# Kernel tuning notes

Measured on AMD Instinct MI355X. Metric: run time of the kernel, lower is better.

The kernel has to match this reference:

```python
import jax, jax.numpy as jnp
import numpy as np

HIDDEN = 128
NUM_FILTERS = 128
NUM_RBF = 50
NUM_LAYERS = 3
MAX_Z = 100
CUTOFF_LO, CUTOFF_HI = 0.0, 5.0
N_ATOMS = 10000
N_EDGES = 320000


def _xavier(k, shape):
    fan_out, fan_in = shape[-2], shape[-1]
    a = (6.0 / (fan_in + fan_out)) ** 0.5
    return jax.random.uniform(k, shape, jnp.float32, -a, a)


def setup_inputs() -> dict:
    key = jax.random.key(0)
    ks = jax.random.split(key, 16)
    start = float(np.exp(-CUTOFF_HI + CUTOFF_LO))  # ExpNormalSmearing start value
    L = NUM_LAYERS
    return {
        "z": jax.random.randint(ks[0], (N_ATOMS,), 0, MAX_Z),
        "edge_index": jax.random.randint(ks[1], (2, N_EDGES), 0, N_ATOMS),
        "edge_weight": jax.random.uniform(ks[2], (N_EDGES,), jnp.float32, 0.0, CUTOFF_HI),
        "emb_table": jax.random.normal(ks[3], (MAX_Z, HIDDEN), jnp.float32),
        "means": jnp.linspace(start, 1.0, NUM_RBF, dtype=jnp.float32),
        "betas": jnp.full((NUM_RBF,), (2.0 / NUM_RBF * (1.0 - start)) ** -2, dtype=jnp.float32),
        "ne_proj_w": _xavier(ks[4], (HIDDEN, NUM_RBF)),
        "ne_proj_b": jnp.zeros((HIDDEN,), jnp.float32),
        "ne_comb_w": _xavier(ks[5], (HIDDEN, 2 * HIDDEN)),
        "ne_comb_b": jnp.zeros((HIDDEN,), jnp.float32),
        "mlp_w0": _xavier(ks[6], (L, NUM_FILTERS, NUM_RBF)),
        "mlp_b0": jnp.zeros((L, NUM_FILTERS), jnp.float32),
        "mlp_w1": _xavier(ks[7], (L, NUM_FILTERS, NUM_FILTERS)),
        "mlp_b1": jnp.zeros((L, NUM_FILTERS), jnp.float32),
        "lin1_w": _xavier(ks[8], (L, NUM_FILTERS, HIDDEN)),
        "lin2_w": _xavier(ks[9], (L, HIDDEN, NUM_FILTERS)),
        "lin2_b": jnp.zeros((L, HIDDEN), jnp.float32),
        "lin_w": _xavier(ks[10], (L, HIDDEN, HIDDEN)),
        "lin_b": jnp.zeros((L, HIDDEN), jnp.float32),
    }


def _cosine_cutoff(d):
    c = 0.5 * (jnp.cos(d * (jnp.pi / CUTOFF_HI)) + 1.0)
    return jnp.where(d < CUTOFF_HI, c, 0.0)


def reference(z, edge_index, edge_weight, emb_table, means, betas,
              ne_proj_w, ne_proj_b, ne_comb_w, ne_comb_b,
              mlp_w0, mlp_b0, mlp_w1, mlp_b1, lin1_w, lin2_w, lin2_b, lin_w, lin_b):
    n_atoms = z.shape[0]
    src, dst = edge_index[0], edge_index[1]
    alpha = 5.0 / (CUTOFF_HI - CUTOFF_LO)
    C = _cosine_cutoff(edge_weight)  # [E]
    # ExpNormalSmearing (includes cutoff factor)
    rbf = jnp.exp(-betas * (jnp.exp(alpha * (CUTOFF_LO - edge_weight))[:, None] - means) ** 2)
    edge_attr = C[:, None] * rbf  # [E, NUM_RBF]

    x = emb_table[z]  # [N, H]

    # NeighborEmbedding (self loops masked out, as in the original)
    mask = (src != dst)[:, None]
    W = (edge_attr @ ne_proj_w.T + ne_proj_b) * C[:, None]
    W = jnp.where(mask, W, 0.0)
    agg = jax.ops.segment_sum(W * emb_table[z][dst], src, num_segments=n_atoms)
    x = jnp.concatenate([x, agg], axis=1) @ ne_comb_w.T + ne_comb_b

    def layer(xc, p):
        w0, b0, w1, b1, l1w, l2w, l2b, lw, lb = p
        # filter network: MLP(edge_attr) * cutoff
        Wf = (jax.nn.silu(edge_attr @ w0.T + b0) @ w1.T + b1) * C[:, None]  # [E, F]
        h = xc @ l1w.T                                   # lin1 (no bias) [N, F]
        a = jax.ops.segment_sum(Wf * h[dst], src, num_segments=n_atoms)  # scatter-add
        h = jax.nn.silu(a @ l2w.T + l2b)                 # lin2 + act
        h = h @ lw.T + lb                                # final linear
        return xc + h, None

    x, _ = jax.lax.scan(layer, x, (mlp_w0, mlp_b0, mlp_w1, mlp_b1, lin1_w, lin2_w, lin2_b, lin_w, lin_b))
    return x
```

## Files before the change

### kernel.cpp

```cpp
#include <hip/hip_runtime.h>
#include <hip/hip_bf16.h>

#define NATOMS 10000
#define NEDGES 320000
#define H 128
#define NRBF 50
#define NELEM (NATOMS * H)
#define NT 4096

typedef unsigned short u16;
typedef unsigned int u32;
typedef __attribute__((ext_vector_type(8))) short short8;
typedef __attribute__((ext_vector_type(4))) float float4v;

__device__ __forceinline__ float bfu(u16 u) { return __uint_as_float(((u32)u) << 16); }
__device__ __forceinline__ u16 bf16r(float v) {
    u32 u = __float_as_uint(v);
    return (u16)((u + 0x7FFFu + ((u >> 16) & 1u)) >> 16);
}
__device__ __forceinline__ float ldf(const void* p, int i, int bf) {
    return bf ? bfu(((const u16*)p)[i]) : ((const float*)p)[i];
}
__device__ __forceinline__ float silu_f(float v) { return v / (1.f + __expf(-v)); }
__device__ __forceinline__ int bfflag(const void* means) {
    return ((((const u32*)means)[24] >> 16) == 0x3F80u) ? 1 : 0;
}

__global__ __launch_bounds__(256) void k_embed(const int* __restrict__ z, const void* emb,
                                               const void* means,
                                               float* __restrict__ x0, u16* __restrict__ xh,
                                               int* __restrict__ degz,
                                               float* __restrict__ zb) {
    int bf = bfflag(means);
    int i = blockIdx.x * 256 + threadIdx.x;
    if (i < 20480) degz[i] = 0;
    if (i < NELEM / 4) ((float4*)zb)[i] = make_float4(0.f, 0.f, 0.f, 0.f);
    if (i < NELEM) {
        int n = i >> 7, f = i & 127;
        float v = ldf(emb, z[n] * H + f, bf);
        x0[i] = v;
        xh[i] = bf16r(v);
    }
}

__device__ __forceinline__ void stage_w16(const void* W, int woff, int wstride,
                                          u16* sW, int tid, int nthr, int bf) {
    u32* sW32 = (u32*)sW;
    if (bf) {
        const u32* W32 = (const u32*)W;
        for (int i = tid; i < 128 * 64; i += nthr) {
            int f2 = i >> 6, kk = i & 63;
            sW32[f2 * 68 + kk] = W32[((woff + f2 * wstride) >> 1) + kk];
        }
    } else {
        const float2* Wf = (const float2*)W;
        for (int i = tid; i < 128 * 64; i += nthr) {
            int f2 = i >> 6, kk = i & 63;
            float2 v = Wf[((woff + f2 * wstride) >> 1) + kk];
            sW32[f2 * 68 + kk] = (u32)bf16r(v.x) | ((u32)bf16r(v.y) << 16);
        }
    }
}

__global__ __launch_bounds__(256) void k_mfma_lin(const float* in,
                                                  const void* W2, int w2off,
                                                  const void* B2, int b2off,
                                                  const void* Wl, int wloff,
                                                  const void* Bl, int bloff,
                                                  const void* W1n, int w1noff,
                                                  float* x, u16* __restrict__ hb,
                                                  const void* means,
                                                  float* zrw, void* outp) {
    __shared__ u16 sW2[128 * 136];
    __shared__ u16 sWl[128 * 136];
    __shared__ u16 sW1[128 * 136];
    __shared__ u16 sA[4][16 * 136];
    __shared__ float sB2v[128], sBlv[128];
    int tid = threadIdx.x;
    int bf = bfflag(means);
    stage_w16(W2, w2off, H, sW2, tid, 256, bf);
    stage_w16(Wl, wloff, H, sWl, tid, 256, bf);
    if (W1n) stage_w16(W1n, w1noff, H, sW1, tid, 256, bf);
    if (tid < 128) {
        sB2v[tid] = ldf(B2, b2off + tid, bf);
        sBlv[tid] = ldf(Bl, bloff + tid, bf);
    }
    __syncthreads();
    int w = tid >> 6, lane = tid & 63;
    int quad = lane >> 4, l16 = lane & 15;
    u16* myA = sA[w];
    u32* myA32 = (u32*)myA;
    for (int tile = blockIdx.x * 4 + w; tile < NATOMS / 16; tile += gridDim.x * 4) {
        int abase = tile * 16;
        const float2* in2 = (const float2*)in + (size_t)abase * 64;
        #pragma unroll 4
        for (int j = 0; j < 16; ++j) {
            float2 v = in2[j * 64 + lane];
            myA32[j * 68 + lane] = (u32)bf16r(v.x) | ((u32)bf16r(v.y) << 16);
        }
        __asm__ volatile("s_waitcnt lgkmcnt(0)" ::: "memory");
        if (zrw) {
            float2* z2 = (float2*)zrw + (size_t)abase * 64;
            #pragma unroll 4
            for (int j = 0; j < 16; ++j) z2[j * 64 + lane] = make_float2(0.f, 0.f);
        }
        short8 af0 = *(const short8*)&myA[l16 * 136 +   0 + quad * 8];
        short8 af1 = *(const short8*)&myA[l16 * 136 +  32 + quad * 8];
        short8 af2 = *(const short8*)&myA[l16 * 136 +  64 + quad * 8];
        short8 af3 = *(const short8*)&myA[l16 * 136 +  96 + quad * 8];
        #pragma unroll 1
        for (int nt = 0; nt < 8; ++nt) {
            const u16* wrow = &sW2[(nt * 16 + l16) * 136];
            short8 b0 = *(const short8*)&wrow[0  + quad * 8];
            short8 b1 = *(const short8*)&wrow[32 + quad * 8];
            short8 b2 = *(const short8*)&wrow[64 + quad * 8];
            short8 b3 = *(const short8*)&wrow[96 + quad * 8];
            float4v acc = {0.f, 0.f, 0.f, 0.f};
            acc = __builtin_amdgcn_mfma_f32_16x16x32_bf16(af0, b0, acc, 0, 0, 0);
            acc = __builtin_amdgcn_mfma_f32_16x16x32_bf16(af1, b1, acc, 0, 0, 0);
            acc = __builtin_amdgcn_mfma_f32_16x16x32_bf16(af2, b2, acc, 0, 0, 0);
            acc = __builtin_amdgcn_mfma_f32_16x16x32_bf16(af3, b3, acc, 0, 0, 0);
            int col = nt * 16 + l16;
            float bias = sB2v[col];
            myA[(quad * 4 + 0) * 136 + col] = bf16r(silu_f(acc[0] + bias));
            myA[(quad * 4 + 1) * 136 + col] = bf16r(silu_f(acc[1] + bias));
            myA[(quad * 4 + 2) * 136 + col] = bf16r(silu_f(acc[2] + bias));
            myA[(quad * 4 + 3) * 136 + col] = bf16r(silu_f(acc[3] + bias));
        }
        __asm__ volatile("s_waitcnt lgkmcnt(0)" ::: "memory");
        short8 t0 = *(const short8*)&myA[l16 * 136 +   0 + quad * 8];
        short8 t1 = *(const short8*)&myA[l16 * 136 +  32 + quad * 8];
        short8 t2 = *(const short8*)&myA[l16 * 136 +  64 + quad * 8];
        short8 t3 = *(const short8*)&myA[l16 * 136 +  96 + quad * 8];
        #pragma unroll 1
        for (int nt = 0; nt < 8; ++nt) {
            const u16* wrow = &sWl[(nt * 16 + l16) * 136];
            short8 b0 = *(const short8*)&wrow[0  + quad * 8];
            short8 b1 = *(const short8*)&wrow[32 + quad * 8];
            short8 b2 = *(const short8*)&wrow[64 + quad * 8];
            short8 b3 = *(const short8*)&wrow[96 + quad * 8];
            int col = nt * 16 + l16;
            float bias = sBlv[col];
            float4v acc;
            acc[0] = x[(size_t)(abase + quad * 4 + 0) * H + col] + bias;
            acc[1] = x[(size_t)(abase + quad * 4 + 1) * H + col] + bias;
            acc[2] = x[(size_t)(abase + quad * 4 + 2) * H + col] + bias;
            acc[3] = x[(size_t)(abase + quad * 4 + 3) * H + col] + bias;
            acc = __builtin_amdgcn_mfma_f32_16x16x32_bf16(t0, b0, acc, 0, 0, 0);
            acc = __builtin_amdgcn_mfma_f32_16x16x32_bf16(t1, b1, acc, 0, 0, 0);
            acc = __builtin_amdgcn_mfma_f32_16x16x32_bf16(t2, b2, acc, 0, 0, 0);
            acc = __builtin_amdgcn_mfma_f32_16x16x32_bf16(t3, b3, acc, 0, 0, 0);
            #pragma unroll
            for (int r = 0; r < 4; ++r) {
                size_t idx = (size_t)(abase + quad * 4 + r) * H + col;
                x[idx] = acc[r];
                myA[(quad * 4 + r) * 136 + col] = bf16r(acc[r]);
                if (outp) {
                    if (bf) ((u16*)outp)[idx] = bf16r(acc[r]);
                    else    ((float*)outp)[idx] = acc[r];
                }
            }
        }
        if (W1n) {
            __asm__ volatile("s_waitcnt lgkmcnt(0)" ::: "memory");
            short8 h0 = *(const short8*)&myA[l16 * 136 +   0 + quad * 8];
            short8 h1 = *(const short8*)&myA[l16 * 136 +  32 + quad * 8];
            short8 h2 = *(const short8*)&myA[l16 * 136 +  64 + quad * 8];
            short8 h3 = *(const short8*)&myA[l16 * 136 +  96 + quad * 8];
            #pragma unroll 1
            for (int nt = 0; nt < 8; ++nt) {
                const u16* wrow = &sW1[(nt * 16 + l16) * 136];
                short8 b0 = *(const short8*)&wrow[0  + quad * 8];
                short8 b1 = *(const short8*)&wrow[32 + quad * 8];
                short8 b2 = *(const short8*)&wrow[64 + quad * 8];
                short8 b3 = *(const short8*)&wrow[96 + quad * 8];
                float4v acc = {0.f, 0.f, 0.f, 0.f};
                acc = __builtin_amdgcn_mfma_f32_16x16x32_bf16(h0, b0, acc, 0, 0, 0);
                acc = __builtin_amdgcn_mfma_f32_16x16x32_bf16(h1, b1, acc, 0, 0, 0);
                acc = __builtin_amdgcn_mfma_f32_16x16x32_bf16(h2, b2, acc, 0, 0, 0);
                acc = __builtin_amdgcn_mfma_f32_16x16x32_bf16(h3, b3, acc, 0, 0, 0);
                int col = nt * 16 + l16;
                hb[(size_t)(abase + quad * 4 + 0) * H + col] = bf16r(acc[0]);
                hb[(size_t)(abase + quad * 4 + 1) * H + col] = bf16r(acc[1]);
                hb[(size_t)(abase + quad * 4 + 2) * H + col] = bf16r(acc[2]);
                hb[(size_t)(abase + quad * 4 + 3) * H + col] = bf16r(acc[3]);
            }
        }
    }
}

__global__ __launch_bounds__(256) void k_mfma_comb(const float* in0, float* in1,
                                                   const void* W, const void* B,
                                                   const void* W1,
                                                   float* x, u16* __restrict__ hb,
                                                   const void* means) {
    __shared__ u16 sWa[128 * 136];
    __shared__ u16 sWb[128 * 136];
    __shared__ u16 sW1[128 * 136];
    __shared__ u16 sA[4][16 * 136];
    __shared__ float sBv[128];
    int tid = threadIdx.x;
    int bf = bfflag(means);
    stage_w16(W, 0,   256, sWa, tid, 256, bf);
    stage_w16(W, 128, 256, sWb, tid, 256, bf);
    stage_w16(W1, 0, H, sW1, tid, 256, bf);
    if (tid < 128) sBv[tid] = ldf(B, tid, bf);
    __syncthreads();
    int w = tid >> 6, lane = tid & 63;
    int quad = lane >> 4, l16 = lane & 15;
    u16* myA = sA[w];
    u32* myA32 = (u32*)myA;
    for (int tile = blockIdx.x * 4 + w; tile < NATOMS / 16; tile += gridDim.x * 4) {
        int abase = tile * 16;
        const float2* i0 = (const float2*)in0 + (size_t)abase * 64;
        const float2* i1 = (const float2*)in1 + (size_t)abase * 64;
        #pragma unroll 4
        for (int j = 0; j < 16; ++j) {
            float2 v = i0[j * 64 + lane];
            myA32[j * 68 + lane] = (u32)bf16r(v.x) | ((u32)bf16r(v.y) << 16);
        }
        __asm__ volatile("s_waitcnt lgkmcnt(0)" ::: "memory");
        short8 af0 = *(const short8*)&myA[l16 * 136 +   0 + quad * 8];
        short8 af1 = *(const short8*)&myA[l16 * 136 +  32 + quad * 8];
        short8 af2 = *(const short8*)&myA[l16 * 136 +  64 + quad * 8];
        short8 af3 = *(const short8*)&myA[l16 * 136 +  96 + quad * 8];
        #pragma unroll 4
        for (int j = 0; j < 16; ++j) {
            float2 v = i1[j * 64 + lane];
            myA32[j * 68 + lane] = (u32)bf16r(v.x) | ((u32)bf16r(v.y) << 16);
        }
        __asm__ volatile("s_waitcnt lgkmcnt(0)" ::: "memory");
        {
            float2* z2 = (float2*)in1 + (size_t)abase * 64;
            #pragma unroll 4
            for (int j = 0; j < 16; ++j) z2[j * 64 + lane] = make_float2(0.f, 0.f);
        }
        short8 ag0 = *(const short8*)&myA[l16 * 136 +   0 + quad * 8];
        short8 ag1 = *(const short8*)&myA[l16 * 136 +  32 + quad * 8];
        short8 ag2 = *(const short8*)&myA[l16 * 136 +  64 + quad * 8];
        short8 ag3 = *(const short8*)&myA[l16 * 136 +  96 + quad * 8];
        #pragma unroll 1
        for (int nt = 0; nt < 8; ++nt) {
            const u16* wra = &sWa[(nt * 16 + l16) * 136];
            const u16* wrb = &sWb[(nt * 16 + l16) * 136];
            int col = nt * 16 + l16;
            float bias = sBv[col];
            float4v acc = {bias, bias, bias, bias};
            acc = __builtin_amdgcn_mfma_f32_16x16x32_bf16(af0, *(const short8*)&wra[0  + quad * 8], acc, 0, 0, 0);
            acc = __builtin_amdgcn_mfma_f32_16x16x32_bf16(af1, *(const short8*)&wra[32 + quad * 8], acc, 0, 0, 0);
            acc = __builtin_amdgcn_mfma_f32_16x16x32_bf16(af2, *(const short8*)&wra[64 + quad * 8], acc, 0, 0, 0);
            acc = __builtin_amdgcn_mfma_f32_16x16x32_bf16(af3, *(const short8*)&wra[96 + quad * 8], acc, 0, 0, 0);
            acc = __builtin_amdgcn_mfma_f32_16x16x32_bf16(ag0, *(const short8*)&wrb[0  + quad * 8], acc, 0, 0, 0);
            acc = __builtin_amdgcn_mfma_f32_16x16x32_bf16(ag1, *(const short8*)&wrb[32 + quad * 8], acc, 0, 0, 0);
            acc = __builtin_amdgcn_mfma_f32_16x16x32_bf16(ag2, *(const short8*)&wrb[64 + quad * 8], acc, 0, 0, 0);
            acc = __builtin_amdgcn_mfma_f32_16x16x32_bf16(ag3, *(const short8*)&wrb[96 + quad * 8], acc, 0, 0, 0);
            #pragma unroll
            for (int r = 0; r < 4; ++r) {
                x[(size_t)(abase + quad * 4 + r) * H + col] = acc[r];
                myA[(quad * 4 + r) * 136 + col] = bf16r(acc[r]);
            }
        }
        __asm__ volatile("s_waitcnt lgkmcnt(0)" ::: "memory");
        short8 h0 = *(const short8*)&myA[l16 * 136 +   0 + quad * 8];
        short8 h1 = *(const short8*)&myA[l16 * 136 +  32 + quad * 8];
        short8 h2 = *(const short8*)&myA[l16 * 136 +  64 + quad * 8];
        short8 h3 = *(const short8*)&myA[l16 * 136 +  96 + quad * 8];
        #pragma unroll 1
        for (int nt = 0; nt < 8; ++nt) {
            const u16* wrow = &sW1[(nt * 16 + l16) * 136];
            short8 b0 = *(const short8*)&wrow[0  + quad * 8];
            short8 b1 = *(const short8*)&wrow[32 + quad * 8];
            short8 b2 = *(const short8*)&wrow[64 + quad * 8];
            short8 b3 = *(const short8*)&wrow[96 + quad * 8];
            float4v acc = {0.f, 0.f, 0.f, 0.f};
            acc = __builtin_amdgcn_mfma_f32_16x16x32_bf16(h0, b0, acc, 0, 0, 0);
            acc = __builtin_amdgcn_mfma_f32_16x16x32_bf16(h1, b1, acc, 0, 0, 0);
            acc = __builtin_amdgcn_mfma_f32_16x16x32_bf16(h2, b2, acc, 0, 0, 0);
            acc = __builtin_amdgcn_mfma_f32_16x16x32_bf16(h3, b3, acc, 0, 0, 0);
            int col = nt * 16 + l16;
            hb[(size_t)(abase + quad * 4 + 0) * H + col] = bf16r(acc[0]);
            hb[(size_t)(abase + quad * 4 + 1) * H + col] = bf16r(acc[1]);
            hb[(size_t)(abase + quad * 4 + 2) * H + col] = bf16r(acc[2]);
            hb[(size_t)(abase + quad * 4 + 3) * H + col] = bf16r(acc[3]);
        }
    }
}

__global__ __launch_bounds__(1024) void k_ft4(const void* means, const void* betas,
                                              const void* W0s, const void* B0s,
                                              const void* W1s, const void* B1s,
                                              const void* Wne, const void* Bne,
                                              u16* __restrict__ ftT,
                                              u16* __restrict__ Tne) {
    __shared__ float sW0[H * 53];
    __shared__ u16 sW1b[128 * 136];
    __shared__ u16 sA16[16 * 136];
    __shared__ float sR[16][56];
    __shared__ float sM[NRBF], sBe[NRBF], sB1v[128], sC[16];
    int tid = threadIdx.x;
    int bf = bfflag(means);
    int t = blockIdx.x >> 8;
    int bb = blockIdx.x & 255;
    int ne = (t == 3);
    const void* W0 = ne ? Wne : W0s;
    int w0off = ne ? 0 : t * H * NRBF;
    u16* T = ne ? Tne : (ftT + (size_t)t * NT * H);
    if (!ne) stage_w16(W1s, t * H * H, H, sW1b, tid, 1024, bf);
    for (int i = tid; i < H * NRBF; i += 1024) {
        int f2 = i / NRBF, k = i - f2 * NRBF;
        sW0[f2 * 53 + k] = ldf(W0, w0off + i, bf);
    }
    if (tid < NRBF) { sM[tid] = ldf(means, tid, bf); sBe[tid] = ldf(betas, tid, bf); }
    if (tid < 128) sB1v[tid] = ne ? 0.f : ldf(B1s, t * H + tid, bf);
    __syncthreads();
    int g = tid >> 7, f = tid & 127;
    float b0r = ne ? ldf(Bne, f, bf) : ldf(B0s, t * H + f, bf);
    int base = bb * 16;
    int n0 = base + 2 * g, n1 = n0 + 1;
    float wv0 = (float)n0 * (5.0f / (NT - 1));
    float wv1 = (float)n1 * (5.0f / (NT - 1));
    if (f < NRBF) {
        float tt = expf(-wv0) - sM[f];
        sR[2 * g][f] = expf(-sBe[f] * tt * tt);
    } else if (f >= 64 && f < 64 + NRBF) {
        float tt = expf(-wv1) - sM[f - 64];
        sR[2 * g + 1][f - 64] = expf(-sBe[f - 64] * tt * tt);
    }
    __syncthreads();
    float c0 = 0.5f * (cosf(wv0 * 0.62831853071795864f) + 1.f); if (!(wv0 < 5.f)) c0 = 0.f;
    float c1 = 0.5f * (cosf(wv1 * 0.62831853071795864f) + 1.f); if (!(wv1 < 5.f)) c1 = 0.f;
    if (f == 0) { sC[2 * g] = c0; sC[2 * g + 1] = c1; }
    float s0 = 0.f, s1 = 0.f;
    #pragma unroll
    for (int k = 0; k < NRBF; ++k) {
        float wk = sW0[f * 53 + k];
        s0 = fmaf(wk, sR[2 * g][k], s0);
        s1 = fmaf(wk, sR[2 * g + 1][k], s1);
    }
    if (ne) {
        T[(size_t)n0 * H + f] = bf16r(fmaf(c0, s0, b0r) * c0);
        T[(size_t)n1 * H + f] = bf16r(fmaf(c1, s1, b0r) * c1);
        return;
    }
    sA16[(2 * g) * 136 + f]     = bf16r(silu_f(fmaf(c0, s0, b0r)));
    sA16[(2 * g + 1) * 136 + f] = bf16r(silu_f(fmaf(c1, s1, b0r)));
    __syncthreads();
    int w = tid >> 6;
    if (w < 8) {
        int lane = tid & 63;
        int quad = lane >> 4, l16 = lane & 15;
        short8 a0 = *(const short8*)&sA16[l16 * 136 +   0 + quad * 8];
        short8 a1 = *(const short8*)&sA16[l16 * 136 +  32 + quad * 8];
        short8 a2 = *(const short8*)&sA16[l16 * 136 +  64 + quad * 8];
        short8 a3 = *(const short8*)&sA16[l16 * 136 +  96 + quad * 8];
        const u16* wrow = &sW1b[(w * 16 + l16) * 136];
        short8 b0 = *(const short8*)&wrow[0  + quad * 8];
        short8 b1 = *(const short8*)&wrow[32 + quad * 8];
        short8 b2 = *(const short8*)&wrow[64 + quad * 8];
        short8 b3 = *(const short8*)&wrow[96 + quad * 8];
        float4v acc = {0.f, 0.f, 0.f, 0.f};
        acc = __builtin_amdgcn_mfma_f32_16x16x32_bf16(a0, b0, acc, 0, 0, 0);
        acc = __builtin_amdgcn_mfma_f32_16x16x32_bf16(a1, b1, acc, 0, 0, 0);
        acc = __builtin_amdgcn_mfma_f32_16x16x32_bf16(a2, b2, acc, 0, 0, 0);
        acc = __builtin_amdgcn_mfma_f32_16x16x32_bf16(a3, b3, acc, 0, 0, 0);
        int col = w * 16 + l16;
        float bias = sB1v[col];
        #pragma unroll
        for (int r = 0; r < 4; ++r) {
            int row = quad * 4 + r;
            T[(size_t)(base + row) * H + col] = bf16r((acc[r] + bias) * sC[row]);
        }
    }
}

__global__ __launch_bounds__(256) void k_hist(const int* __restrict__ src, int* __restrict__ deg) {
    int e = blockIdx.x * 256 + threadIdx.x;
    if (e < NEDGES) atomicAdd(&deg[src[e]], 1);
}

__global__ __launch_bounds__(1024) void k_scan(const int* __restrict__ deg, int* __restrict__ rs) {
    __shared__ int wsum[16];
    int tid = threadIdx.x;
    int lane = tid & 63, w = tid >> 6;
    int d[10];
    int tot = 0;
    int base_i = tid * 10;
    if (tid < 1000) {
        #pragma unroll
        for (int j = 0; j < 10; ++j) d[j] = deg[base_i + j];
        #pragma unroll
        for (int j = 0; j < 10; ++j) { int v = d[j]; d[j] = tot; tot += v; }
    }
    int inc = tot;
    #pragma unroll
    for (int off = 1; off < 64; off <<= 1) {
        int n = __shfl_up(inc, off, 64);
        if (lane >= off) inc += n;
    }
    if (lane == 63) wsum[w] = inc;
    __syncthreads();
    if (w == 0) {
        int v = (lane < 16) ? wsum[lane] : 0;
        int vinc = v;
        #pragma unroll
        for (int off = 1; off < 16; off <<= 1) {
            int n = __shfl_up(vinc, off, 64);
            if (lane >= off) vinc += n;
        }
        if (lane < 16) wsum[lane] = vinc - v;
    }
    __syncthreads();
    if (tid < 1000) {
        int base = wsum[w] + (inc - tot);
        #pragma unroll
        for (int j = 0; j < 10; ++j) rs[base_i + j] = base + d[j];
    }
}

__global__ __launch_bounds__(256) void k_scatter_perm(const int* __restrict__ src,
                                                      const int* __restrict__ dst,
                                                      const void* ew, const void* means,
                                                      const int* __restrict__ rs,
                                                      int* __restrict__ cnt,
                                                      u32* __restrict__ sds,
                                                      float* __restrict__ ews) {
    int bf = bfflag(means);
    int e = blockIdx.x * 256 + threadIdx.x;
    if (e < NEDGES) {
        int s = src[e];
        int p = rs[s] + atomicAdd(&cnt[s], 1);
        sds[p] = (u32)s | ((u32)dst[e] << 14);
        ews[p] = ldf(ew, e, bf) * ((float)(NT - 1) / 5.0f);
    }
}

#define ELOAD(i) \
    u32 sd##i = sds[e + i]; \
    int s##i = (int)(sd##i & 16383u), d##i = (int)(sd##i >> 14); \
    float u##i = ews[e + i]; \
    int ix##i = min((int)u##i, NT - 2); float fr##i = u##i - (float)ix##i; \
    u32 ta##i = Tb[ix##i * 64 + lane], tb##i = Tb[ix##i * 64 + 64 + lane]; \
    u32 h##i = vh[d##i * 64 + lane];
#define EVAL(i) \
    float vx##i = fmaf(fr##i, bfu((u16)(tb##i & 0xffff)) - bfu((u16)(ta##i & 0xffff)), bfu((u16)(ta##i & 0xffff))) * bfu((u16)(h##i & 0xffff)); \
    float vy##i = fmaf(fr##i, bfu((u16)(tb##i >> 16))    - bfu((u16)(ta##i >> 16)),    bfu((u16)(ta##i >> 16)))    * bfu((u16)(h##i >> 16));
#define EACC(i) \
    if (!(mask_self && s##i == d##i)) { \
        if (s##i != cur) { \
            if (cur >= 0) { atomicAdd(&acc[cur * H + 2 * lane], rx); atomicAdd(&acc[cur * H + 2 * lane + 1], ry); } \
            cur = s##i; rx = 0.f; ry = 0.f; \
        } \
        rx += vx##i; ry += vy##i; \
    }

__global__ __launch_bounds__(256) void k_edge_apply4(const u32* __restrict__ sds,
                                                     const float* __restrict__ ews,
                                                     const u32* __restrict__ Tb,
                                                     const u32* __restrict__ vh,
                                                     float* __restrict__ acc,
                                                     int mask_self) {
    int tid = threadIdx.x;
    int g = tid >> 6;
    int lane = tid & 63;
    int gid = blockIdx.x * 4 + g;
    int r0 = gid * 40;
    int cur = -1;
    float rx = 0.f, ry = 0.f;
    for (int e = r0; e < r0 + 40; e += 8) {
        ELOAD(0) ELOAD(1) ELOAD(2) ELOAD(3) ELOAD(4) ELOAD(5) ELOAD(6) ELOAD(7)
        EVAL(0) EVAL(1) EVAL(2) EVAL(3) EVAL(4) EVAL(5) EVAL(6) EVAL(7)
        EACC(0) EACC(1) EACC(2) EACC(3) EACC(4) EACC(5) EACC(6) EACC(7)
    }
    if (cur >= 0) {
        atomicAdd(&acc[cur * H + 2 * lane], rx);
        atomicAdd(&acc[cur * H + 2 * lane + 1], ry);
    }
}

extern "C" void kernel_launch(void* const* d_in, const int* in_sizes, int n_in,
                              void* d_out, int out_size, void* d_ws, size_t ws_size,
                              hipStream_t stream) {
    const int* z  = (const int*)d_in[0];
    const int* ei = (const int*)d_in[1];
    const void* ew        = d_in[2];
    const void* emb       = d_in[3];
    const void* means     = d_in[4];
    const void* betas     = d_in[5];
    const void* ne_proj_w = d_in[6];
    const void* ne_proj_b = d_in[7];
    const void* ne_comb_w = d_in[8];
    const void* ne_comb_b = d_in[9];
    const void* mlp_w0    = d_in[10];
    const void* mlp_b0    = d_in[11];
    const void* mlp_w1    = d_in[12];
    const void* mlp_b1    = d_in[13];
    const void* lin1_w    = d_in[14];
    const void* lin2_w    = d_in[15];
    const void* lin2_b    = d_in[16];
    const void* lin_w     = d_in[17];
    const void* lin_b     = d_in[18];

    const int* srcp = ei;
    const int* dstp = ei + NEDGES;

    float* buf0 = (float*)d_ws;
    float* buf1 = buf0 + NELEM;
    float* x    = buf1 + NELEM;
    int*   deg  = (int*)(x + NELEM);
    int*   cnt  = deg + 10240;
    int*   rs   = cnt + 10240;
    u32*   sds  = (u32*)(rs + 10240);
    float* ews  = (float*)(sds + NEDGES);
    u16*   Tb   = (u16*)(ews + NEDGES);
    u16*   hb   = Tb + NT * H;
    u16*   ftT  = hb + NELEM;

    const int gElem = (NELEM + 255) / 256;
    const int gEdge = (NEDGES + 255) / 256;

    k_embed<<<gElem, 256, 0, stream>>>(z, emb, means, buf0, hb, deg, buf1);

    k_hist<<<gEdge, 256, 0, stream>>>(srcp, deg);
    k_scan<<<1, 1024, 0, stream>>>(deg, rs);
    k_scatter_perm<<<gEdge, 256, 0, stream>>>(srcp, dstp, ew, means, rs, cnt,
                                              sds, ews);

    k_ft4<<<1024, 1024, 0, stream>>>(means, betas, mlp_w0, mlp_b0, mlp_w1, mlp_b1,
                                     ne_proj_w, ne_proj_b, ftT, Tb);

    k_edge_apply4<<<2000, 256, 0, stream>>>(sds, ews, (const u32*)Tb,
                                            (const u32*)hb, buf1, 1);
    k_mfma_comb<<<157, 256, 0, stream>>>(buf0, buf1, ne_comb_w, ne_comb_b,
                                         lin1_w, x, hb, means);

    for (int L = 0; L < 3; ++L) {
        k_edge_apply4<<<2000, 256, 0, stream>>>(sds, ews,
                                                (const u32*)(ftT + (size_t)L * NT * H),
                                                (const u32*)hb, buf1, 0);
        k_mfma_lin<<<157, 256, 0, stream>>>(buf1, lin2_w, L * H * H, lin2_b, L * H,
                                            lin_w, L * H * H, lin_b, L * H,
                                            (L < 2) ? lin1_w : nullptr, (L + 1) * H * H,
                                            x, hb, means,
                                            (L < 2) ? buf1 : nullptr,
                                            (L == 2) ? d_out : nullptr);
    }
}
```

Baseline: 344.3 us.

## Replace atomic edge scatter with per-atom CSR gather writing bf16 aggregates

The edge kernel now assigns one wavefront per source atom and walks that atom's CSR segment, accumulating in registers and writing the result once. This replaces the fixed 40-edge chunks that flushed with float atomicAdds. The aggregate is stored directly as packed bf16, so the MFMA kernels copy it straight into shared memory with no conversion and no longer need to zero the buffer. Edge records are packed into a single uint2 (dst, scaled weight). In exchange, work per wavefront now depends on atom degree and can be unbalanced, and there is no parallelism inside an atom.

```diff
diff --git a/kernel.cpp b/kernel.cpp
--- a/kernel.cpp
+++ b/kernel.cpp
@@ -29,12 +29,10 @@
 __global__ __launch_bounds__(256) void k_embed(const int* __restrict__ z, const void* emb,
                                                const void* means,
                                                float* __restrict__ x0, u16* __restrict__ xh,
-                                               int* __restrict__ degz,
-                                               float* __restrict__ zb) {
+                                               int* __restrict__ degz) {
     int bf = bfflag(means);
     int i = blockIdx.x * 256 + threadIdx.x;
     if (i < 20480) degz[i] = 0;
-    if (i < NELEM / 4) ((float4*)zb)[i] = make_float4(0.f, 0.f, 0.f, 0.f);
     if (i < NELEM) {
         int n = i >> 7, f = i & 127;
         float v = ldf(emb, z[n] * H + f, bf);
@@ -62,7 +60,7 @@
     }
 }
 
-__global__ __launch_bounds__(256) void k_mfma_lin(const float* in,
+__global__ __launch_bounds__(256) void k_mfma_lin(const u32* __restrict__ in,
                                                   const void* W2, int w2off,
                                                   const void* B2, int b2off,
                                                   const void* Wl, int wloff,
@@ -70,7 +68,7 @@
                                                   const void* W1n, int w1noff,
                                                   float* x, u16* __restrict__ hb,
                                                   const void* means,
-                                                  float* zrw, void* outp) {
+                                                  void* outp) {
     __shared__ u16 sW2[128 * 136];
     __shared__ u16 sWl[128 * 136];
     __shared__ u16 sW1[128 * 136];
@@ -92,18 +90,11 @@
     u32* myA32 = (u32*)myA;
     for (int tile = blockIdx.x * 4 + w; tile < NATOMS / 16; tile += gridDim.x * 4) {
         int abase = tile * 16;
-        const float2* in2 = (const float2*)in + (size_t)abase * 64;
+        const u32* in2 = in + (size_t)abase * 64;
         #pragma unroll 4
-        for (int j = 0; j < 16; ++j) {
-            float2 v = in2[j * 64 + lane];
-            myA32[j * 68 + lane] = (u32)bf16r(v.x) | ((u32)bf16r(v.y) << 16);
-        }
+        for (int j = 0; j < 16; ++j)
+            myA32[j * 68 + lane] = in2[j * 64 + lane];
         __asm__ volatile("s_waitcnt lgkmcnt(0)" ::: "memory");
-        if (zrw) {
-            float2* z2 = (float2*)zrw + (size_t)abase * 64;
-            #pragma unroll 4
-            for (int j = 0; j < 16; ++j) z2[j * 64 + lane] = make_float2(0.f, 0.f);
-        }
         short8 af0 = *(const short8*)&myA[l16 * 136 +   0 + quad * 8];
         short8 af1 = *(const short8*)&myA[l16 * 136 +  32 + quad * 8];
         short8 af2 = *(const short8*)&myA[l16 * 136 +  64 + quad * 8];
@@ -189,7 +180,7 @@
     }
 }
 
-__global__ __launch_bounds__(256) void k_mfma_comb(const float* in0, float* in1,
+__global__ __launch_bounds__(256) void k_mfma_comb(const float* in0, const u32* __restrict__ in1,
                                                    const void* W, const void* B,
                                                    const void* W1,
                                                    float* x, u16* __restrict__ hb,
@@ -213,7 +204,7 @@
     for (int tile = blockIdx.x * 4 + w; tile < NATOMS / 16; tile += gridDim.x * 4) {
         int abase = tile * 16;
         const float2* i0 = (const float2*)in0 + (size_t)abase * 64;
-        const float2* i1 = (const float2*)in1 + (size_t)abase * 64;
+        const u32* i1 = in1 + (size_t)abase * 64;
         #pragma unroll 4
         for (int j = 0; j < 16; ++j) {
             float2 v = i0[j * 64 + lane];
@@ -225,16 +216,9 @@
         short8 af2 = *(const short8*)&myA[l16 * 136 +  64 + quad * 8];
         short8 af3 = *(const short8*)&myA[l16 * 136 +  96 + quad * 8];
         #pragma unroll 4
-        for (int j = 0; j < 16; ++j) {
-            float2 v = i1[j * 64 + lane];
-            myA32[j * 68 + lane] = (u32)bf16r(v.x) | ((u32)bf16r(v.y) << 16);
-        }
+        for (int j = 0; j < 16; ++j)
+            myA32[j * 68 + lane] = i1[j * 64 + lane];
         __asm__ volatile("s_waitcnt lgkmcnt(0)" ::: "memory");
-        {
-            float2* z2 = (float2*)in1 + (size_t)abase * 64;
-            #pragma unroll 4
-            for (int j = 0; j < 16; ++j) z2[j * 64 + lane] = make_float2(0.f, 0.f);
-        }
         short8 ag0 = *(const short8*)&myA[l16 * 136 +   0 + quad * 8];
         short8 ag1 = *(const short8*)&myA[l16 * 136 +  32 + quad * 8];
         short8 ag2 = *(const short8*)&myA[l16 * 136 +  64 + quad * 8];
@@ -422,59 +406,57 @@
                                                       const void* ew, const void* means,
                                                       const int* __restrict__ rs,
                                                       int* __restrict__ cnt,
-                                                      u32* __restrict__ sds,
-                                                      float* __restrict__ ews) {
+                                                      uint2* __restrict__ ed) {
     int bf = bfflag(means);
     int e = blockIdx.x * 256 + threadIdx.x;
     if (e < NEDGES) {
         int s = src[e];
         int p = rs[s] + atomicAdd(&cnt[s], 1);
-        sds[p] = (u32)s | ((u32)dst[e] << 14);
-        ews[p] = ldf(ew, e, bf) * ((float)(NT - 1) / 5.0f);
-    }
-}
-
-#define ELOAD(i) \
-    u32 sd##i = sds[e + i]; \
-    int s##i = (int)(sd##i & 16383u), d##i = (int)(sd##i >> 14); \
-    float u##i = ews[e + i]; \
+        float u = ldf(ew, e, bf) * ((float)(NT - 1) / 5.0f);
+        ed[p] = make_uint2((u32)dst[e], __float_as_uint(u));
+    }
+}
+
+#define GEV(i) \
+    uint2 ed##i = ed[e + i]; \
+    int d##i = (int)ed##i.x; float u##i = __uint_as_float(ed##i.y); \
     int ix##i = min((int)u##i, NT - 2); float fr##i = u##i - (float)ix##i; \
     u32 ta##i = Tb[ix##i * 64 + lane], tb##i = Tb[ix##i * 64 + 64 + lane]; \
-    u32 h##i = vh[d##i * 64 + lane];
-#define EVAL(i) \
+    u32 h##i = vh[d##i * 64 + lane]; \
     float vx##i = fmaf(fr##i, bfu((u16)(tb##i & 0xffff)) - bfu((u16)(ta##i & 0xffff)), bfu((u16)(ta##i & 0xffff))) * bfu((u16)(h##i & 0xffff)); \
     float vy##i = fmaf(fr##i, bfu((u16)(tb##i >> 16))    - bfu((u16)(ta##i >> 16)),    bfu((u16)(ta##i >> 16)))    * bfu((u16)(h##i >> 16));
-#define EACC(i) \
-    if (!(mask_self && s##i == d##i)) { \
-        if (s##i != cur) { \
-            if (cur >= 0) { atomicAdd(&acc[cur * H + 2 * lane], rx); atomicAdd(&acc[cur * H + 2 * lane + 1], ry); } \
-            cur = s##i; rx = 0.f; ry = 0.f; \
-        } \
-        rx += vx##i; ry += vy##i; \
-    }
-
-__global__ __launch_bounds__(256) void k_edge_apply4(const u32* __restrict__ sds,
-                                                     const float* __restrict__ ews,
+#define GACC(i) \
+    if (!(mask_self && d##i == s)) { rx += vx##i; ry += vy##i; }
+
+__global__ __launch_bounds__(256) void k_edge_gather(const int* __restrict__ rs,
+                                                     const uint2* __restrict__ ed,
                                                      const u32* __restrict__ Tb,
                                                      const u32* __restrict__ vh,
-                                                     float* __restrict__ acc,
+                                                     u32* __restrict__ accb,
                                                      int mask_self) {
     int tid = threadIdx.x;
-    int g = tid >> 6;
-    int lane = tid & 63;
-    int gid = blockIdx.x * 4 + g;
-    int r0 = gid * 40;
-    int cur = -1;
+    int g = tid >> 6, lane = tid & 63;
+    int s = blockIdx.x * 4 + g;
+    if (s >= NATOMS) return;
+    int e0 = rs[s];
+    int e1 = (s < NATOMS - 1) ? rs[s + 1] : NEDGES;
     float rx = 0.f, ry = 0.f;
-    for (int e = r0; e < r0 + 40; e += 8) {
-        ELOAD(0) ELOAD(1) ELOAD(2) ELOAD(3) ELOAD(4) ELOAD(5) ELOAD(6) ELOAD(7)
-        EVAL(0) EVAL(1) EVAL(2) EVAL(3) EVAL(4) EVAL(5) EVAL(6) EVAL(7)
-        EACC(0) EACC(1) EACC(2) EACC(3) EACC(4) EACC(5) EACC(6) EACC(7)
-    }
-    if (cur >= 0) {
-        atomicAdd(&acc[cur * H + 2 * lane], rx);
-        atomicAdd(&acc[cur * H + 2 * lane + 1], ry);
-    }
+    int e = e0;
+    for (; e + 8 <= e1; e += 8) {
+        GEV(0) GEV(1) GEV(2) GEV(3) GEV(4) GEV(5) GEV(6) GEV(7)
+        GACC(0) GACC(1) GACC(2) GACC(3) GACC(4) GACC(5) GACC(6) GACC(7)
+    }
+    for (; e < e1; ++e) {
+        uint2 edt = ed[e];
+        int dt = (int)edt.x; float ut = __uint_as_float(edt.y);
+        int ixt = min((int)ut, NT - 2); float frt = ut - (float)ixt;
+        u32 tat = Tb[ixt * 64 + lane], tbt = Tb[ixt * 64 + 64 + lane];
+        u32 ht = vh[dt * 64 + lane];
+        float vxt = fmaf(frt, bfu((u16)(tbt & 0xffff)) - bfu((u16)(tat & 0xffff)), bfu((u16)(tat & 0xffff))) * bfu((u16)(ht & 0xffff));
+        float vyt = fmaf(frt, bfu((u16)(tbt >> 16))    - bfu((u16)(tat >> 16)),    bfu((u16)(tat >> 16)))    * bfu((u16)(ht >> 16));
+        if (!(mask_self && dt == s)) { rx += vxt; ry += vyt; }
+    }
+    accb[(size_t)s * 64 + lane] = (u32)bf16r(rx) | ((u32)bf16r(ry) << 16);
 }
 
 extern "C" void kernel_launch(void* const* d_in, const int* in_sizes, int n_in,
@@ -504,44 +486,41 @@
     const int* dstp = ei + NEDGES;
 
     float* buf0 = (float*)d_ws;
-    float* buf1 = buf0 + NELEM;
-    float* x    = buf1 + NELEM;
-    int*   deg  = (int*)(x + NELEM);
+    float* x    = buf0 + NELEM;
+    u32*   accb = (u32*)(x + NELEM);
+    int*   deg  = (int*)(accb + NELEM / 2);
     int*   cnt  = deg + 10240;
     int*   rs   = cnt + 10240;
-    u32*   sds  = (u32*)(rs + 10240);
-    float* ews  = (float*)(sds + NEDGES);
-    u16*   Tb   = (u16*)(ews + NEDGES);
+    uint2* ed   = (uint2*)(rs + 10240);
+    u16*   Tb   = (u16*)(ed + NEDGES);
     u16*   hb   = Tb + NT * H;
     u16*   ftT  = hb + NELEM;
 
     const int gElem = (NELEM + 255) / 256;
     const int gEdge = (NEDGES + 255) / 256;
 
-    k_embed<<<gElem, 256, 0, stream>>>(z, emb, means, buf0, hb, deg, buf1);
+    k_embed<<<gElem, 256, 0, stream>>>(z, emb, means, buf0, hb, deg);
 
     k_hist<<<gEdge, 256, 0, stream>>>(srcp, deg);
     k_scan<<<1, 1024, 0, stream>>>(deg, rs);
-    k_scatter_perm<<<gEdge, 256, 0, stream>>>(srcp, dstp, ew, means, rs, cnt,
-                                              sds, ews);
+    k_scatter_perm<<<gEdge, 256, 0, stream>>>(srcp, dstp, ew, means, rs, cnt, ed);
 
     k_ft4<<<1024, 1024, 0, stream>>>(means, betas, mlp_w0, mlp_b0, mlp_w1, mlp_b1,
                                      ne_proj_w, ne_proj_b, ftT, Tb);
 
-    k_edge_apply4<<<2000, 256, 0, stream>>>(sds, ews, (const u32*)Tb,
-                                            (const u32*)hb, buf1, 1);
-    k_mfma_comb<<<157, 256, 0, stream>>>(buf0, buf1, ne_comb_w, ne_comb_b,
+    k_edge_gather<<<2500, 256, 0, stream>>>(rs, ed, (const u32*)Tb,
+                                            (const u32*)hb, accb, 1);
+    k_mfma_comb<<<157, 256, 0, stream>>>(buf0, accb, ne_comb_w, ne_comb_b,
                                          lin1_w, x, hb, means);
 
     for (int L = 0; L < 3; ++L) {
-        k_edge_apply4<<<2000, 256, 0, stream>>>(sds, ews,
+        k_edge_gather<<<2500, 256, 0, stream>>>(rs, ed,
                                                 (const u32*)(ftT + (size_t)L * NT * H),
-                                                (const u32*)hb, buf1, 0);
-        k_mfma_lin<<<157, 256, 0, stream>>>(buf1, lin2_w, L * H * H, lin2_b, L * H,
+                                                (const u32*)hb, accb, 0);
+        k_mfma_lin<<<157, 256, 0, stream>>>(accb, lin2_w, L * H * H, lin2_b, L * H,
                                             lin_w, L * H * H, lin_b, L * H,
                                             (L < 2) ? lin1_w : nullptr, (L + 1) * H * H,
                                             x, hb, means,
-                                            (L < 2) ? buf1 : nullptr,
                                             (L == 2) ? d_out : nullptr);
     }
 }
```

Result: faster. 331.2 us (-3.8%).
